# Kernel tuning notes

Measured on AMD Instinct MI355X. Metric: run time of the kernel, lower is better.

The kernel has to match this reference:

```python
import jax, jax.numpy as jnp
import numpy as np

B, N, DIM = 4, 1024, 512
DEPTH, HEADS, DH = 4, 8, 64
INNER = HEADS * DH  # 512
W = 32              # sqrt(N), FeedForward reshapes tokens to (W, W)
SCALE = DH ** -0.5  # used for BOTH spatial and spectral branches (as in source)
EPS_LN = 1e-5
EPS_BN = 1e-5


def setup_inputs() -> dict:
    key = jax.random.key(0)
    ks = jax.random.split(key, 16)
    L = DEPTH
    def rn(k, shape, s=0.02):
        return jax.random.normal(k, shape, jnp.float32) * s
    return {
        "x": jax.random.normal(ks[0], (B, N, DIM), jnp.float32),
        "ln1_w": jnp.ones((L, DIM), jnp.float32), "ln1_b": jnp.zeros((L, DIM), jnp.float32),
        "Wqkv": rn(ks[1], (L, DIM, 3 * INNER)),
        "Wout": rn(ks[2], (L, INNER, DIM)), "bout": jnp.zeros((L, DIM), jnp.float32),
        "sp_w": rn(ks[3], (L, HEADS, HEADS, 3, 3), 0.1), "sp_b": jnp.zeros((L, HEADS), jnp.float32),
        "Wqkv_spec": rn(ks[4], (L, N, 3 * N)),
        "spec_w": rn(ks[5], (L, 1, 1, 3, 3), 0.1), "spec_b": jnp.zeros((L, 1), jnp.float32),
        "ln2_w": jnp.ones((L, DIM), jnp.float32), "ln2_b": jnp.zeros((L, DIM), jnp.float32),
        "dw_w": rn(ks[6], (L, DIM, 1, 3, 3), 0.1), "dw_b": jnp.zeros((L, DIM), jnp.float32),
        "pw_w": rn(ks[7], (L, 256, DIM)), "pw_b": jnp.zeros((L, 256), jnp.float32),
        "bn_g": jnp.ones((L, 256), jnp.float32), "bn_b": jnp.zeros((L, 256), jnp.float32),
        "bn_m": jnp.zeros((L, 256), jnp.float32), "bn_v": jnp.ones((L, 256), jnp.float32),
        "c1_w": rn(ks[8], (L, 512, 256)), "c1_b": jnp.zeros((L, 512), jnp.float32),
        "c2_w": rn(ks[9], (L, DIM, 512)), "c2_b": jnp.zeros((L, DIM), jnp.float32),
    }


def _ln(x, w, b):
    mu = x.mean(-1, keepdims=True)
    var = x.var(-1, keepdims=True)  # biased, matching torch LayerNorm
    return (x - mu) * jax.lax.rsqrt(var + EPS_LN) * w + b


def _conv3x3(x, w, b, groups=1):
    y = jax.lax.conv_general_dilated(x, w, (1, 1), 'SAME',
                                     dimension_numbers=('NCHW', 'OIHW', 'NCHW'),
                                     feature_group_count=groups)
    return y + b[None, :, None, None]


def _block(x, p):
    (ln1w, ln1b, Wqkv, Wout, bout, spw, spb, Wqs, scw, scb,
     ln2w, ln2b, dww, dwb, pww, pwb, bng, bnb, bnm, bnv, c1w, c1b, c2w, c2b) = p
    b = x.shape[0]
    # --- spatial attention (PreNorm) ---
    h = _ln(x, ln1w, ln1b)
    q, k, v = jnp.split(h @ Wqkv, 3, axis=-1)
    split_heads = lambda t: t.reshape(b, N, HEADS, DH).transpose(0, 2, 1, 3)  # b h n d
    q, k, v = split_heads(q), split_heads(k), split_heads(v)
    attn = jax.nn.softmax(jnp.einsum('bhid,bhjd->bhij', q, k) * SCALE, axis=-1)
    attn = _conv3x3(attn, spw, spb)  # conv over the softmax map (heads as channels)
    out = jnp.einsum('bhij,bhjd->bhid', attn, v).transpose(0, 2, 1, 3).reshape(b, N, INNER)
    out = out @ Wout + bout  # (b, n, dim)
    # --- spectral attention on h^T (b, dim, n); v_spec is dead code in source ---
    xt = jnp.swapaxes(h, -1, -2)
    qs, ks_, _vs = jnp.split(xt @ Wqs, 3, axis=-1)  # each (b, dim, n)
    a = jax.nn.softmax(jnp.einsum('bin,bjn->bij', qs, ks_) * SCALE, axis=-1)
    a = _conv3x3(a[:, None], scw, scb)[:, 0]  # (b, dim, dim)
    x = x + jnp.einsum('bnd,bde->bne', out, a)  # residual add from Transformer loop
    # --- FeedForward (PreNorm), FF adds its own internal residual too ---
    h2 = _ln(x, ln2w, ln2b)
    img = h2.reshape(b, W, W, DIM).transpose(0, 3, 1, 2)  # 'b (w h) c -> b c w h'
    t = _conv3x3(img, dww, dwb, groups=DIM)               # depthwise 3x3
    t = jnp.einsum('oc,bchw->bohw', pww, t) + pwb[None, :, None, None]  # pointwise dim->256
    t = (t - bnm[None, :, None, None]) * jax.lax.rsqrt(bnv + EPS_BN)[None, :, None, None] \
        * bng[None, :, None, None] + bnb[None, :, None, None]           # BatchNorm2d (eval)
    t = jax.nn.gelu(jnp.einsum('oc,bchw->bohw', c1w, t) + c1b[None, :, None, None], approximate=False)
    t = jax.nn.gelu(jnp.einsum('oc,bchw->bohw', c2w, t) + c2b[None, :, None, None], approximate=False)
    ff = h2 + t.transpose(0, 2, 3, 1).reshape(b, N, DIM)  # FF internal residual
    return x + ff


def _forward(x, ln1_w, ln1_b, Wqkv, Wout, bout, sp_w, sp_b, Wqkv_spec, spec_w, spec_b,
             ln2_w, ln2_b, dw_w, dw_b, pw_w, pw_b, bn_g, bn_b, bn_m, bn_v,
             c1_w, c1_b, c2_w, c2_b):
    stacked = (ln1_w, ln1_b, Wqkv, Wout, bout, sp_w, sp_b, Wqkv_spec, spec_w, spec_b,
               ln2_w, ln2_b, dw_w, dw_b, pw_w, pw_b, bn_g, bn_b, bn_m, bn_v,
               c1_w, c1_b, c2_w, c2_b)
    for i in range(DEPTH):
        x = _block(x, tuple(a[i] for a in stacked))
    return x


def reference(x, ln1_w, ln1_b, Wqkv, Wout, bout, sp_w, sp_b, Wqkv_spec, spec_w, spec_b,
              ln2_w, ln2_b, dw_w, dw_b, pw_w, pw_b, bn_g, bn_b, bn_m, bn_v,
              c1_w, c1_b, c2_w, c2_b):
    return _forward(x, ln1_w, ln1_b, Wqkv, Wout, bout, sp_w, sp_b, Wqkv_spec, spec_w, spec_b,
                    ln2_w, ln2_b, dw_w, dw_b, pw_w, pw_b, bn_g, bn_b, bn_m, bn_v,
                    c1_w, c1_b, c2_w, c2_b)
```

## Files before the change

kernel.cpp:

```cpp
#include <hip/hip_runtime.h>
#include <hip/hip_bf16.h>

typedef __hip_bfloat16 bf16;
typedef __attribute__((ext_vector_type(8))) short bf16x8;
typedef __attribute__((ext_vector_type(4))) float f32x4;

__device__ __forceinline__ float b2f(bf16 v){ return __bfloat162float(v); }
__device__ __forceinline__ bf16 f2b(float v){ return __float2bfloat16(v); }
__device__ __forceinline__ float bits2f(unsigned u){ return __uint_as_float(u << 16); }
__device__ __forceinline__ unsigned short f2bits(float v){ bf16 t = __float2bfloat16(v); return *(unsigned short*)&t; }

__device__ __forceinline__ float gelu_f(float x){
  return 0.5f * x * (1.f + erff(x * 0.7071067811865475f));
}

__device__ __forceinline__ void gload_lds(const void* g, void* l){
  __builtin_amdgcn_global_load_lds((const __attribute__((address_space(1))) void*)g,
                                   (__attribute__((address_space(3))) void*)l, 16, 0, 0);
}

template<bool MAX>
__device__ __forceinline__ float block_reduce(float v){
  __shared__ float s[4];
  #pragma unroll
  for (int o = 32; o > 0; o >>= 1){
    float t = __shfl_down(v, o, 64);
    v = MAX ? fmaxf(v, t) : (v + t);
  }
  int lane = threadIdx.x & 63, w = threadIdx.x >> 6;
  __syncthreads();
  if (lane == 0) s[w] = v;
  __syncthreads();
  return MAX ? fmaxf(fmaxf(s[0], s[1]), fmaxf(s[2], s[3]))
             : (s[0] + s[1] + s[2] + s[3]);
}

__global__ void detect_k(const unsigned* __restrict__ x, int* __restrict__ flag){
  __shared__ int cnt[256];
  int tid = threadIdx.x;
  int c = 0;
  for (int i = tid; i < 4096; i += 256){
    unsigned h = x[i] & 0xffffu;
    int e = (int)((h >> 7) & 0xff);
    if (h == 0u || (e >= 100 && e <= 133)) c++;
  }
  cnt[tid] = c;
  __syncthreads();
  for (int o = 128; o > 0; o >>= 1){ if (tid < o) cnt[tid] += cnt[tid+o]; __syncthreads(); }
  if (tid == 0) *flag = (cnt[0] < 2048) ? 1 : 0;
}

__global__ __launch_bounds__(256) void cvt_x_k(const void* __restrict__ src,
                                               float* __restrict__ X,
                                               const int* __restrict__ flag){
  int p = blockIdx.x*256 + threadIdx.x;
  X[p] = (*flag) ? ((const float*)src)[p]
                 : __bfloat162float(((const bf16*)src)[p]);
}

struct WCvt21 { const void* src[21]; long long cum[22]; };

__global__ __launch_bounds__(256) void cvt_w_k(WCvt21 a, bf16* __restrict__ WB,
                                               long long total, const int* __restrict__ flag){
  long long i = (long long)blockIdx.x*256 + threadIdx.x;
  if (i >= total) return;
  int t = 0;
  while (a.cum[t+1] <= i) t++;
  long long e = i - a.cum[t];
  WB[i] = (*flag) ? __float2bfloat16(((const float*)a.src[t])[e])
                  : ((const bf16*)a.src[t])[e];
}

__global__ __launch_bounds__(256) void wtrans_k(const void* __restrict__ src, bf16* __restrict__ dst,
                                                int ld_src, int ldd, long long sSrc, long long sDst,
                                                const int* __restrict__ flag){
  __shared__ bf16 t[64][65];
  int z = blockIdx.z;
  int r0 = blockIdx.x*64, c0 = blockIdx.y*64;
  int lane = threadIdx.x & 63, quad = threadIdx.x >> 6;
  const float* sf = (const float*)src;
  const bf16* sb = (const bf16*)src;
  int fl = *flag;
  #pragma unroll
  for (int k = 0; k < 16; ++k){
    int r = quad*16 + k;
    long long idx = z*sSrc + (long long)(r0+r)*ld_src + c0 + lane;
    float v = fl ? sf[idx] : b2f(sb[idx]);
    t[r][lane] = f2b(v);
  }
  __syncthreads();
  #pragma unroll
  for (int k = 0; k < 16; ++k){
    int c = quad*16 + k;
    dst[z*sDst + (long long)(c0+c)*ldd + r0 + lane] = t[lane][c];
  }
}

__global__ void wprep_k(const bf16* __restrict__ spw, bf16* __restrict__ Wr){
  int l = blockIdx.x;
  for (int t = threadIdx.x; t < 1536; t += 256){
    int ho = t / 96, k = t - ho*96;
    float v = 0.f;
    if (ho < 8 && k < 72){
      int tap = k >> 3, hi = k & 7;
      v = b2f(spw[l*576 + ho*72 + hi*9 + tap]);
    }
    Wr[l*1536 + t] = f2b(v);
  }
}

__global__ __launch_bounds__(256) void store_out_k(const float* __restrict__ X,
                                                   void* __restrict__ out,
                                                   const int* __restrict__ flag){
  int p = blockIdx.x*256 + threadIdx.x;
  if (*flag) ((float*)out)[p] = X[p];
  else       ((bf16*)out)[p] = f2b(X[p]);
}

template<int MF, int NF, typename TC>
__global__ __launch_bounds__(256) void gmfma_k(
    int M, int N, int K,
    const bf16* __restrict__ A, int lda, long long sA, long long sA2,
    const bf16* __restrict__ Bt, int ldb, long long sB, long long sB2,
    TC* __restrict__ C, int ldc, long long sC, long long sC2,
    float alpha, int beta,
    const bf16* __restrict__ bias_n,
    const float* __restrict__ scale_n,
    const float* __restrict__ shift_n,
    const bf16* __restrict__ addF,
    int act,
    bf16* __restrict__ vt)
{
  constexpr int BM = MF*32, BN = NF*32;
  constexpr int CHA = BM/16, CH = (BM+BN)/16;
  static_assert(CH % 4 == 0, "chunks must divide among 4 waves");
  __shared__ bf16 Asm[BM][32];
  __shared__ bf16 Bsm[BN][32];
  const int tid = threadIdx.x;
  const int lane = tid & 63, wid = tid >> 6;
  const int wm = wid >> 1, wn = wid & 1;
  const int m0 = blockIdx.y*BM, n0 = blockIdx.x*BN;
  const int z = blockIdx.z;
  const long long zl = z & 7, zh = z >> 3;
  const bf16* Ab = A + zl*sA + zh*sA2;
  const bf16* Bb = Bt + zl*sB + zh*sB2;
  TC* Cb = C + zl*sC + zh*sC2;
  const bf16* Fb = addF ? addF + zl*sC + zh*sC2 : nullptr;

  f32x4 acc[MF][NF];
  f32x4 zero = {0.f, 0.f, 0.f, 0.f};
  #pragma unroll
  for (int m = 0; m < MF; ++m)
    #pragma unroll
    for (int n = 0; n < NF; ++n) acc[m][n] = zero;

  const int rchunk = lane >> 2;
  const int kchunk = (lane & 3) * 8;
  const int row16 = lane & 15, kq = (lane >> 4) * 8;

  for (int k0 = 0; k0 < K; k0 += 32){
    #pragma unroll
    for (int cc = 0; cc < CH/4; ++cc){
      int c = wid + cc*4;
      if (c < CHA){
        int row = c*16 + rchunk;
        gload_lds(Ab + (long long)(m0+row)*lda + k0 + kchunk, &Asm[c*16][0]);
      } else {
        int row = (c-CHA)*16 + rchunk;
        gload_lds(Bb + (long long)(n0+row)*ldb + k0 + kchunk, &Bsm[(c-CHA)*16][0]);
      }
    }
    __syncthreads();
    bf16x8 af[MF], bfr[NF];
    #pragma unroll
    for (int m = 0; m < MF; ++m)
      af[m] = *(const bf16x8*)&Asm[wm*(MF*16) + m*16 + row16][kq];
    #pragma unroll
    for (int n = 0; n < NF; ++n)
      bfr[n] = *(const bf16x8*)&Bsm[wn*(NF*16) + n*16 + row16][kq];
    #pragma unroll
    for (int m = 0; m < MF; ++m)
      #pragma unroll
      for (int n = 0; n < NF; ++n)
        acc[m][n] = __builtin_amdgcn_mfma_f32_16x16x32_bf16(af[m], bfr[n], acc[m][n], 0, 0, 0);
    __syncthreads();
  }

  #pragma unroll
  for (int m = 0; m < MF; ++m){
    #pragma unroll
    for (int n = 0; n < NF; ++n){
      int gn = n0 + wn*(NF*16) + n*16 + row16;
      float bn_ = bias_n ? b2f(bias_n[gn]) : 0.f;
      float sc = scale_n ? scale_n[gn] : 1.f;
      float sh = shift_n ? shift_n[gn] : 0.f;
      int gmb = m0 + wm*(MF*16) + m*16 + (lane >> 4)*4;
      float vals[4];
      #pragma unroll
      for (int r = 0; r < 4; ++r){
        int gm = gmb + r;
        float v = acc[m][n][r] * alpha + bn_;
        v = v * sc + sh;
        if (act) v = gelu_f(v);
        long long idx = (long long)gm*ldc + gn;
        if (Fb) v += b2f(Fb[idx]);
        if (beta){
          float old;
          if constexpr (__is_same(TC, float)) old = Cb[idx]; else old = b2f(Cb[idx]);
          v += old;
        }
        if constexpr (__is_same(TC, float)) Cb[idx] = v; else Cb[idx] = f2b(v);
        vals[r] = v;
      }
      if (vt && gn >= 1024){
        int h = (gn - 1024) >> 6, d = (gn - 1024) & 63;
        int bb = gmb >> 10, nn = gmb & 1023;
        ushort4 o;
        o.x = f2bits(vals[0]); o.y = f2bits(vals[1]);
        o.z = f2bits(vals[2]); o.w = f2bits(vals[3]);
        *(ushort4*)&vt[(((long long)bb*8 + h)*64 + d)*1024 + nn] = o;
      }
    }
  }
}

template<int MF, int NF, typename TC>
static void gmfma_x(hipStream_t st, int z, int M, int N, int K,
                    const bf16* A, int lda, long long sA, long long sA2,
                    const bf16* Bt, int ldb, long long sB, long long sB2,
                    TC* C, int ldc, long long sC, long long sC2,
                    float alpha = 1.f, int beta = 0,
                    const bf16* bias_n = nullptr,
                    const float* scale_n = nullptr, const float* shift_n = nullptr,
                    const bf16* addF = nullptr, int act = 0, bf16* vt = nullptr)
{
  dim3 g(N/(NF*32), M/(MF*32), z);
  gmfma_k<MF,NF,TC><<<g, 256, 0, st>>>(M,N,K,A,lda,sA,sA2,Bt,ldb,sB,sB2,C,ldc,sC,sC2,
                                       alpha,beta,bias_n,scale_n,shift_n,addF,act,vt);
}

template<int MF, int NF, typename TC>
static void gmfma(hipStream_t st, int z, int M, int N, int K,
                  const bf16* A, int lda, long long sA,
                  const bf16* Bt, int ldb, long long sB,
                  TC* C, int ldc, long long sC,
                  float alpha = 1.f, int beta = 0,
                  const bf16* bias_n = nullptr,
                  const float* scale_n = nullptr, const float* shift_n = nullptr,
                  const bf16* addF = nullptr, int act = 0, bf16* vt = nullptr)
{
  gmfma_x<MF,NF,TC>(st, z, M, N, K, A, lda, sA, 8*sA, Bt, ldb, sB, 8*sB,
                    C, ldc, sC, 8*sC, alpha, beta, bias_n, scale_n, shift_n, addF, act, vt);
}

__global__ __launch_bounds__(256) void ln_k(const float* __restrict__ X, bf16* __restrict__ Y,
                                            const bf16* __restrict__ w, const bf16* __restrict__ b){
  long long row = blockIdx.x;
  const float* x = X + row*512;
  bf16* y = Y + row*512;
  int tid = threadIdx.x;
  float v0 = x[tid], v1 = x[tid+256];
  float mean = block_reduce<false>(v0+v1) * (1.f/512.f);
  float msq  = block_reduce<false>(v0*v0+v1*v1) * (1.f/512.f);
  float var = msq - mean*mean;
  float rs = rsqrtf(var + 1e-5f);
  y[tid]     = f2b((v0-mean)*rs*b2f(w[tid])     + b2f(b[tid]));
  y[tid+256] = f2b((v1-mean)*rs*b2f(w[tid+256]) + b2f(b[tid+256]));
}

__global__ __launch_bounds__(256) void maxsum_k(const bf16* __restrict__ Sp,
                                                float* __restrict__ Mrow, float* __restrict__ Irow,
                                                long long bstride){
  __shared__ float redmx[4][8];
  __shared__ float redsum[4][8];
  int i = blockIdx.x;
  long long b = blockIdx.y;
  const bf16* src = Sp + b*bstride + (long long)i*1024;
  int tid = threadIdx.x;
  int lane = tid & 63, w = tid >> 6;
  int j0 = tid*4;

  float v[8][4];
  #pragma unroll
  for (int h = 0; h < 8; ++h){
    ushort4 u = *(const ushort4*)&src[h*1048576 + j0];
    v[h][0] = bits2f(u.x); v[h][1] = bits2f(u.y);
    v[h][2] = bits2f(u.z); v[h][3] = bits2f(u.w);
  }
  #pragma unroll
  for (int h = 0; h < 8; ++h){
    float m = fmaxf(fmaxf(v[h][0], v[h][1]), fmaxf(v[h][2], v[h][3]));
    #pragma unroll
    for (int o = 32; o > 0; o >>= 1) m = fmaxf(m, __shfl_xor(m, o, 64));
    if (lane == 0) redmx[w][h] = m;
  }
  __syncthreads();
  float mx[8];
  #pragma unroll
  for (int h = 0; h < 8; ++h)
    mx[h] = fmaxf(fmaxf(redmx[0][h], redmx[1][h]), fmaxf(redmx[2][h], redmx[3][h]));
  #pragma unroll
  for (int h = 0; h < 8; ++h){
    float s = 0.f;
    #pragma unroll
    for (int r = 0; r < 4; ++r) s += __expf(v[h][r] - mx[h]);
    #pragma unroll
    for (int o = 32; o > 0; o >>= 1) s += __shfl_xor(s, o, 64);
    if (lane == 0) redsum[w][h] = s;
  }
  __syncthreads();
  if (tid < 8){
    float s = redsum[0][tid] + redsum[1][tid] + redsum[2][tid] + redsum[3][tid];
    long long o = (b*1024 + i)*8 + tid;
    Mrow[o] = mx[tid];
    Irow[o] = 1.f / s;
  }
}

__device__ __forceinline__ int csw(int col){ return col ^ ((col >> 3) & 7); }

__global__ __launch_bounds__(256) void convNorm_k(
    const bf16* __restrict__ Sp, bf16* __restrict__ Pout,
    const bf16* __restrict__ Wr, const bf16* __restrict__ bias,
    const float* __restrict__ Mrow, const float* __restrict__ Irow,
    long long bstride)
{
  __shared__ bf16 tile[10][66][8];
  __shared__ float mrow[10][8];
  __shared__ float irow[10][8];
  long long b = blockIdx.z;
  int i0 = blockIdx.y*8;
  int jh0 = blockIdx.x*512;
  int tid = threadIdx.x;
  const bf16* src = Sp + b*bstride;

  if (tid < 80){
    int r = tid >> 3, h = tid & 7;
    int gi = i0 + r - 1;
    float m = 0.f, iv = 0.f;
    if ((unsigned)gi < 1024u){ long long o = (b*1024 + gi)*8 + h; m = Mrow[o]; iv = Irow[o]; }
    mrow[r][h] = m; irow[r][h] = iv;
  }

  int lane = tid & 63, wid = tid >> 6;
  int row16 = lane & 15, q = lane >> 4;
  bf16x8 wf0 = *(const bf16x8*)&Wr[row16*96 +  0 + q*8];
  bf16x8 wf1 = *(const bf16x8*)&Wr[row16*96 + 32 + q*8];
  bf16x8 wf2 = *(const bf16x8*)&Wr[row16*96 + 64 + q*8];
  float bv = (row16 < 8) ? b2f(bias[row16]) : 0.f;

  for (int c = 0; c < 8; ++c){
    int base = jh0 + c*64;
    __syncthreads();
    for (int t = tid; t < 320; t += 256){
      int row = t >> 5, rem = t & 31;
      int hp = rem >> 3, seg = rem & 7;
      int gi = i0 + row - 1;
      int g0 = base + seg*8;
      unsigned ov[8];
      if ((unsigned)gi < 1024u){
        const bf16* p0 = src + (long long)(2*hp)*1048576 + (long long)gi*1024 + g0;
        bf16x8 a0 = *(const bf16x8*)p0;
        bf16x8 a1 = *(const bf16x8*)(p0 + 1048576);
        float m0 = mrow[row][2*hp],   i0v = irow[row][2*hp];
        float m1 = mrow[row][2*hp+1], i1v = irow[row][2*hp+1];
        #pragma unroll
        for (int k = 0; k < 8; ++k){
          float e0 = __expf(bits2f((unsigned)(unsigned short)a0[k]) - m0) * i0v;
          float e1 = __expf(bits2f((unsigned)(unsigned short)a1[k]) - m1) * i1v;
          ov[k] = (unsigned)f2bits(e0) | ((unsigned)f2bits(e1) << 16);
        }
      } else {
        #pragma unroll
        for (int k = 0; k < 8; ++k) ov[k] = 0u;
      }
      #pragma unroll
      for (int k = 0; k < 8; ++k)
        *(unsigned*)&tile[row][csw(1 + seg*8 + k)][2*hp] = ov[k];
    }
    if (tid < 40){
      int row = tid >> 2, hp = tid & 3;
      int gi = i0 + row - 1;
      unsigned L = 0u, R = 0u;
      if ((unsigned)gi < 1024u){
        long long rb = (long long)gi*1024;
        int cl = base - 1, cr = base + 64;
        float m0 = mrow[row][2*hp],   i0v = irow[row][2*hp];
        float m1 = mrow[row][2*hp+1], i1v = irow[row][2*hp+1];
        if (cl >= 0){
          float e0 = __expf(b2f(src[(long long)(2*hp)*1048576 + rb + cl]) - m0) * i0v;
          float e1 = __expf(b2f(src[(long long)(2*hp+1)*1048576 + rb + cl]) - m1) * i1v;
          L = (unsigned)f2bits(e0) | ((unsigned)f2bits(e1) << 16);
        }
        if (cr < 1024){
          float e0 = __expf(b2f(src[(long long)(2*hp)*1048576 + rb + cr]) - m0) * i0v;
          float e1 = __expf(b2f(src[(long long)(2*hp+1)*1048576 + rb + cr]) - m1) * i1v;
          R = (unsigned)f2bits(e0) | ((unsigned)f2bits(e1) << 16);
        }
      }
      *(unsigned*)&tile[row][csw(0)][2*hp] = L;
      *(unsigned*)&tile[row][csw(65)][2*hp] = R;
    }
    __syncthreads();
    #pragma unroll
    for (int rr = 0; rr < 2; ++rr){
      int ii = rr*4 + wid;
      f32x4 zero = {0.f,0.f,0.f,0.f};
      f32x4 acc[4] = {zero,zero,zero,zero};
      #pragma unroll
      for (int ks = 0; ks < 3; ++ks){
        int tap = ks*4 + q;
        int tcl = tap > 8 ? 0 : tap;
        int di = tcl/3, dj = tcl - di*3;
        bf16x8 wsel = ks==0 ? wf0 : (ks==1 ? wf1 : wf2);
        #pragma unroll
        for (int mf = 0; mf < 4; ++mf){
          bf16x8 af = *(const bf16x8*)&tile[ii+di][csw(mf*16 + row16 + dj)][0];
          acc[mf] = __builtin_amdgcn_mfma_f32_16x16x32_bf16(af, wsel, acc[mf], 0, 0, 0);
        }
      }
      if (row16 < 8){
        bf16* dst = Pout + b*bstride + (long long)row16*1048576 + (long long)(i0+ii)*1024;
        #pragma unroll
        for (int mf = 0; mf < 4; ++mf){
          int j = base + mf*16 + q*4;
          ushort4 o;
          o.x = f2bits(acc[mf][0] + bv);
          o.y = f2bits(acc[mf][1] + bv);
          o.z = f2bits(acc[mf][2] + bv);
          o.w = f2bits(acc[mf][3] + bv);
          *(ushort4*)&dst[j] = o;
        }
      }
    }
  }
}

__global__ __launch_bounds__(256) void spec_ms_k(const float* __restrict__ A,
                                                 float* __restrict__ Sm, float* __restrict__ Si){
  int row = blockIdx.x;
  const float* p = A + (long long)row*512;
  int tid = threadIdx.x;
  float v0 = p[tid], v1 = p[tid+256];
  float mx = block_reduce<true>(fmaxf(v0, v1));
  float s = block_reduce<false>(__expf(v0-mx) + __expf(v1-mx));
  if (tid == 0){ Sm[row] = mx; Si[row] = 1.f/s; }
}

__global__ __launch_bounds__(256) void conv_spec_k(const float* __restrict__ in, bf16* __restrict__ out,
                                                   const bf16* __restrict__ w, const bf16* __restrict__ bias,
                                                   const float* __restrict__ Sm, const float* __restrict__ Si){
  __shared__ float ti[66][67];
  __shared__ bf16 toutT[64][65];
  __shared__ float sms[66], sis[66];
  int b = blockIdx.z;
  int i0 = blockIdx.y*64, j0 = blockIdx.x*64;
  int tid = threadIdx.x;
  const float* ib = in + (long long)b*262144;
  if (tid < 66){
    int gi = i0 + tid - 1;
    float m = 0.f, iv = 0.f;
    if ((unsigned)gi < 512u){ m = Sm[b*512 + gi]; iv = Si[b*512 + gi]; }
    sms[tid] = m; sis[tid] = iv;
  }
  __syncthreads();
  for (int t = tid; t < 66*66; t += 256){
    int r = t / 66, cc = t - r*66;
    int gi = i0 + r - 1, gj = j0 + cc - 1;
    float v = 0.f;
    if ((unsigned)gi < 512u && (unsigned)gj < 512u)
      v = __expf(ib[gi*512 + gj] - sms[r]) * sis[r];
    ti[r][cc] = v;
  }
  __syncthreads();
  float w9[9], bv = b2f(bias[0]);
  #pragma unroll
  for (int d = 0; d < 9; ++d) w9[d] = b2f(w[d]);
  int ii = tid & 63;
  #pragma unroll
  for (int q = 0; q < 16; ++q){
    int jj = (tid >> 6)*16 + q;
    float acc = bv;
    #pragma unroll
    for (int di = 0; di < 3; ++di)
      #pragma unroll
      for (int dj = 0; dj < 3; ++dj)
        acc += w9[di*3+dj] * ti[ii+di][jj+dj];
    toutT[jj][ii] = f2b(acc);
  }
  __syncthreads();
  #pragma unroll
  for (int q = 0; q < 16; ++q){
    int jj = (tid >> 6)*16 + q;
    out[(long long)b*262144 + (j0+jj)*512 + i0 + (tid & 63)] = toutT[jj][tid & 63];
  }
}

__global__ __launch_bounds__(256) void dwconv_k(const bf16* __restrict__ H2, bf16* __restrict__ T1,
                                                const bf16* __restrict__ w, const bf16* __restrict__ bias){
  int p = blockIdx.x*256 + threadIdx.x;
  int cp = p & 255;
  int n = (p >> 8) & 1023;
  int b = p >> 18;
  int c0 = cp*2;
  int wi = n >> 5, hg = n & 31;
  float a0 = b2f(bias[c0]), a1 = b2f(bias[c0+1]);
  #pragma unroll
  for (int di = 0; di < 3; ++di){
    int gw = wi + di - 1;
    if ((unsigned)gw >= 32u) continue;
    #pragma unroll
    for (int dj = 0; dj < 3; ++dj){
      int gh = hg + dj - 1;
      if ((unsigned)gh >= 32u) continue;
      unsigned hv = *(const unsigned*)&H2[((long long)b*1024 + (gw*32+gh))*512 + c0];
      float w0 = b2f(w[c0*9 + di*3 + dj]);
      float w1 = b2f(w[(c0+1)*9 + di*3 + dj]);
      a0 += w0 * bits2f(hv & 0xffffu);
      a1 += w1 * bits2f(hv >> 16);
    }
  }
  bf16 h0 = f2b(a0), h1 = f2b(a1);
  unsigned o = ((unsigned)*(unsigned short*)&h1 << 16) | (unsigned)*(unsigned short*)&h0;
  *(unsigned*)&T1[((long long)b*1024 + n)*512 + c0] = o;
}

__global__ void bnaff_all_k(const bf16* __restrict__ pwb, const bf16* __restrict__ g,
                            const bf16* __restrict__ bb, const bf16* __restrict__ m,
                            const bf16* __restrict__ v, float* __restrict__ BNAFF){
  int l = blockIdx.x, o = threadIdx.x;
  float s = b2f(g[l*256+o]) * rsqrtf(b2f(v[l*256+o]) + 1e-5f);
  BNAFF[l*512 + o] = s;
  BNAFF[l*512 + 256 + o] = (b2f(pwb[l*256+o]) - b2f(m[l*256+o])) * s + b2f(bb[l*256+o]);
}

__global__ __launch_bounds__(256) void htrans_k(const bf16* __restrict__ Hb, bf16* __restrict__ HT){
  __shared__ bf16 t[64][65];
  int b = blockIdx.z;
  int n0 = blockIdx.x*64, c0 = blockIdx.y*64;
  int lane = threadIdx.x & 63, quad = threadIdx.x >> 6;
  #pragma unroll
  for (int k = 0; k < 16; ++k){
    int r = quad*16 + k;
    t[r][lane] = Hb[((long long)b*1024 + n0 + r)*512 + c0 + lane];
  }
  __syncthreads();
  #pragma unroll
  for (int k = 0; k < 16; ++k){
    int c = quad*16 + k;
    HT[(long long)b*524288 + (long long)(c0+c)*1024 + n0 + lane] = t[lane][c];
  }
}

extern "C" void kernel_launch(void* const* d_in, const int* in_sizes, int n_in,
                              void* d_out, int out_size, void* d_ws, size_t ws_size,
                              hipStream_t stream)
{
  (void)in_sizes; (void)n_in; (void)out_size;

  const bool big = ws_size >= 207000000ull;
  const long long ATTN_SZ = big ? 33554432LL : 8388608LL;

  float* X     = (float*)d_ws;
  bf16*  WBsm  = (bf16*)(X + 2097152);
  bf16*  WqkvT = WBsm  + 2139648;
  bf16*  WoutT = WqkvT + 3145728;
  bf16*  WqsT  = WoutT + 1048576;
  bf16*  Hbuf  = WqsT  + 8388608;
  bf16*  HbufT = Hbuf  + 2097152;
  bf16*  QKV   = HbufT + 2097152;
  bf16*  Vt    = QKV   + 6291456;
  bf16*  OUTH  = Vt    + 2097152;
  bf16*  OUT   = OUTH  + 2097152;
  bf16*  ATTN  = OUT   + 2097152;
  bf16*  ATTNC = ATTN  + ATTN_SZ;
  float* BNAFF = (float*)(ATTNC + ATTN_SZ);
  bf16*  WR    = (bf16*)(BNAFF + 2048);
  float* MROW  = (float*)(WR + 6144);
  float* IROW  = MROW + 32768;
  float* SMS   = IROW + 32768;
  float* SIS   = SMS + 2048;
  int*   FLAG  = (int*)(SIS + 2048);

  float* ASPEC   = (float*)OUTH;
  bf16*  ASPECCT = ATTNC;
  bf16*  T1 = ATTN;
  bf16*  T3 = ATTN + 2097152;
  bf16*  T2 = ATTNC + 2097152;
  bf16*  SQK = ATTN;

  static const int widx[21] = {1,2,5,6,7,9,10,11,12,13,14,15,16,17,18,19,20,21,22,23,24};
  static const long long wsz[21] = {2048,2048,2048,2304,32,36,4,2048,2048,18432,2048,
                                    524288,1024,1024,1024,1024,1024,524288,2048,1048576,2048};
  WCvt21 wc;
  long long cum = 0;
  bf16* wp[21];
  for (int t = 0; t < 21; ++t){
    wc.src[t] = d_in[widx[t]];
    wc.cum[t] = cum;
    wp[t] = WBsm + cum;
    cum += wsz[t];
  }
  wc.cum[21] = cum;

  bf16 *w_ln1w = wp[0],  *w_ln1b = wp[1],  *w_bout = wp[2],  *w_spw = wp[3];
  bf16 *w_spb  = wp[4],  *w_specw= wp[5],  *w_specb= wp[6],  *w_ln2w= wp[7];
  bf16 *w_ln2b = wp[8],  *w_dww  = wp[9],  *w_dwb  = wp[10], *w_pww = wp[11];
  bf16 *w_pwb  = wp[12], *w_bng  = wp[13], *w_bnb  = wp[14], *w_bnm = wp[15];
  bf16 *w_bnv  = wp[16], *w_c1w  = wp[17], *w_c1b  = wp[18], *w_c2w = wp[19];
  bf16 *w_c2b  = wp[20];

  detect_k<<<1, 256, 0, stream>>>((const unsigned*)d_in[0], FLAG);
  cvt_x_k<<<8192, 256, 0, stream>>>(d_in[0], X, FLAG);
  cvt_w_k<<<(int)((cum + 255)/256), 256, 0, stream>>>(wc, WBsm, cum, FLAG);
  wtrans_k<<<dim3(8,24,4), 256, 0, stream>>>(d_in[3], WqkvT, 1536, 512, 786432LL, 786432LL, FLAG);
  wtrans_k<<<dim3(8, 8,4), 256, 0, stream>>>(d_in[4], WoutT,  512, 512, 262144LL, 262144LL, FLAG);
  wtrans_k<<<dim3(16,32,4),256, 0, stream>>>(d_in[8], WqsT,  3072,1024, 3145728LL,2097152LL, FLAG);
  bnaff_all_k<<<4, 256, 0, stream>>>(w_pwb, w_bng, w_bnb, w_bnm, w_bnv, BNAFF);
  wprep_k<<<4, 256, 0, stream>>>(w_spw, WR);

  for (int l = 0; l < 4; ++l){
    ln_k<<<4096, 256, 0, stream>>>(X, Hbuf, w_ln1w + l*512, w_ln1b + l*512);
    gmfma<4,4,bf16>(stream, 1, 4096, 1536, 512,
        Hbuf, 512, 0, WqkvT + (long long)l*786432, 512, 0, QKV, 1536, 0,
        1.f, 0, nullptr, nullptr, nullptr, nullptr, 0, Vt);
    if (big){
      gmfma_x<4,4,bf16>(stream, 32, 1024, 1024, 64,
          QKV, 1536, 64, 1572864, QKV + 512, 1536, 64, 1572864,
          ATTN, 1024, 1048576, 8388608, 0.125f);
      maxsum_k<<<dim3(1024,4), 256, 0, stream>>>(ATTN, MROW, IROW, 8388608LL);
      convNorm_k<<<dim3(2,128,4), 256, 0, stream>>>(ATTN, ATTNC, WR + l*1536, w_spb + l*8,
                                                    MROW, IROW, 8388608LL);
      gmfma_x<2,2,bf16>(stream, 32, 1024, 64, 1024,
          ATTNC, 1024, 1048576, 8388608, Vt, 1024, 65536, 524288,
          OUTH, 512, 64, 524288);
    } else {
      for (int b = 0; b < 4; ++b){
        bf16* qkvb = QKV + (long long)b*1572864;
        gmfma<4,4,bf16>(stream, 8, 1024, 1024, 64,
            qkvb, 1536, 64, qkvb + 512, 1536, 64, ATTN, 1024, 1048576, 0.125f);
        maxsum_k<<<dim3(1024,1), 256, 0, stream>>>(ATTN, MROW, IROW, 8388608LL);
        convNorm_k<<<dim3(2,128,1), 256, 0, stream>>>(ATTN, ATTNC, WR + l*1536, w_spb + l*8,
                                                      MROW, IROW, 8388608LL);
        gmfma<2,2,bf16>(stream, 8, 1024, 64, 1024,
            ATTNC, 1024, 1048576, Vt + (long long)b*524288, 1024, 65536,
            OUTH + (long long)b*524288, 512, 64);
      }
    }
    gmfma<2,2,bf16>(stream, 1, 4096, 512, 512,
        OUTH, 512, 0, WoutT + (long long)l*262144, 512, 0, OUT, 512, 0,
        1.f, 0, w_bout + l*512);
    htrans_k<<<dim3(16,8,4), 256, 0, stream>>>(Hbuf, HbufT);
    gmfma<4,4,bf16>(stream, 4, 512, 2048, 1024,
        HbufT, 1024, 524288, WqsT + (long long)l*2097152, 1024, 0, SQK, 2048, 1048576);
    gmfma<2,2,float>(stream, 4, 512, 512, 1024,
        SQK, 2048, 1048576, SQK + 1024, 2048, 1048576, ASPEC, 512, 262144, 0.125f);
    spec_ms_k<<<2048, 256, 0, stream>>>(ASPEC, SMS, SIS);
    conv_spec_k<<<dim3(8,8,4), 256, 0, stream>>>(ASPEC, ASPECCT, w_specw + l*9, w_specb + l,
                                                 SMS, SIS);
    gmfma<2,2,float>(stream, 4, 1024, 512, 512,
        OUT, 512, 524288, ASPECCT, 512, 262144, X, 512, 524288, 1.f, 1);
    ln_k<<<4096, 256, 0, stream>>>(X, Hbuf, w_ln2w + l*512, w_ln2b + l*512);
    dwconv_k<<<4096, 256, 0, stream>>>(Hbuf, T1, w_dww + l*4608, w_dwb + l*512);
    gmfma<2,2,bf16>(stream, 4, 1024, 256, 512,
        T1, 512, 524288, w_pww + (long long)l*131072, 512, 0, T2, 256, 262144,
        1.f, 0, nullptr, BNAFF + l*512, BNAFF + l*512 + 256);
    gmfma<2,2,bf16>(stream, 4, 1024, 512, 256,
        T2, 256, 262144, w_c1w + (long long)l*131072, 256, 0, T3, 512, 524288,
        1.f, 0, w_c1b + l*512, nullptr, nullptr, nullptr, 1);
    gmfma<2,2,float>(stream, 4, 1024, 512, 512,
        T3, 512, 524288, w_c2w + (long long)l*262144, 512, 0, X, 512, 524288,
        1.f, 1, w_c2b + l*512, nullptr, nullptr, Hbuf, 1);
  }

  store_out_k<<<8192, 256, 0, stream>>>(X, d_out, FLAG);
}
```

Measured before the change: 1.233 ms.

## Fuse softmax exp and row-sum into score GEMM epilogue, drop max-sum kernels

The score GEMMs for both spatial and spectral attention now apply exp in their epilogue, store the exponentials, and atomically accumulate per-row sums. This removes the separate max/sum reduction kernels and the exp in the conv-normalize kernels, which now just multiply by the reciprocal row sum. The max subtraction is dropped, so correctness relies on scores being small enough not to overflow exp. It adds atomics, a zeroing kernel each layer, and regrids convNorm to more blocks.

```diff
diff --git a/kernel.cpp b/kernel.cpp
--- a/kernel.cpp
+++ b/kernel.cpp
@@ -117,7 +117,12 @@
   else       ((bf16*)out)[p] = f2b(X[p]);
 }
 
-template<int MF, int NF, typename TC>
+__global__ __launch_bounds__(256) void zero_k(float* __restrict__ p, int n){
+  int i = blockIdx.x*256 + threadIdx.x;
+  if (i < n) p[i] = 0.f;
+}
+
+template<int MF, int NF, typename TC, int EXP>
 __global__ __launch_bounds__(256) void gmfma_k(
     int M, int N, int K,
     const bf16* __restrict__ A, int lda, long long sA, long long sA2,
@@ -129,7 +134,8 @@
     const float* __restrict__ shift_n,
     const bf16* __restrict__ addF,
     int act,
-    bf16* __restrict__ vt)
+    bf16* __restrict__ vt,
+    float* __restrict__ srow, long long szl, long long szh, long long sgm)
 {
   constexpr int BM = MF*32, BN = NF*32;
   constexpr int CHA = BM/16, CH = (BM+BN)/16;
@@ -184,6 +190,34 @@
       for (int n = 0; n < NF; ++n)
         acc[m][n] = __builtin_amdgcn_mfma_f32_16x16x32_bf16(af[m], bfr[n], acc[m][n], 0, 0, 0);
     __syncthreads();
+  }
+
+  if constexpr (EXP){
+    #pragma unroll
+    for (int m = 0; m < MF; ++m){
+      int gmb = m0 + wm*(MF*16) + m*16 + (lane >> 4)*4;
+      float rowsum[4] = {0.f, 0.f, 0.f, 0.f};
+      #pragma unroll
+      for (int n = 0; n < NF; ++n){
+        int gn = n0 + wn*(NF*16) + n*16 + row16;
+        #pragma unroll
+        for (int r = 0; r < 4; ++r){
+          float e = __expf(acc[m][n][r] * alpha);
+          long long idx = (long long)(gmb + r)*ldc + gn;
+          if constexpr (__is_same(TC, float)) Cb[idx] = e; else Cb[idx] = f2b(e);
+          rowsum[r] += e;
+        }
+      }
+      #pragma unroll
+      for (int r = 0; r < 4; ++r){
+        float s = rowsum[r];
+        #pragma unroll
+        for (int o = 1; o < 16; o <<= 1) s += __shfl_xor(s, o, 64);
+        if ((lane & 15) == 0)
+          atomicAdd(&srow[zl*szl + zh*szh + (long long)(gmb + r)*sgm], s);
+      }
+    }
+    return;
   }
 
   #pragma unroll
@@ -235,8 +269,9 @@
                     const bf16* addF = nullptr, int act = 0, bf16* vt = nullptr)
 {
   dim3 g(N/(NF*32), M/(MF*32), z);
-  gmfma_k<MF,NF,TC><<<g, 256, 0, st>>>(M,N,K,A,lda,sA,sA2,Bt,ldb,sB,sB2,C,ldc,sC,sC2,
-                                       alpha,beta,bias_n,scale_n,shift_n,addF,act,vt);
+  gmfma_k<MF,NF,TC,0><<<g, 256, 0, st>>>(M,N,K,A,lda,sA,sA2,Bt,ldb,sB,sB2,C,ldc,sC,sC2,
+                                         alpha,beta,bias_n,scale_n,shift_n,addF,act,vt,
+                                         nullptr,0,0,0);
 }
 
 template<int MF, int NF, typename TC>
@@ -251,6 +286,20 @@
 {
   gmfma_x<MF,NF,TC>(st, z, M, N, K, A, lda, sA, 8*sA, Bt, ldb, sB, 8*sB,
                     C, ldc, sC, 8*sC, alpha, beta, bias_n, scale_n, shift_n, addF, act, vt);
+}
+
+template<int MF, int NF, typename TC>
+static void gmfma_exp(hipStream_t st, int z, int M, int N, int K,
+                      const bf16* A, int lda, long long sA, long long sA2,
+                      const bf16* Bt, int ldb, long long sB, long long sB2,
+                      TC* C, int ldc, long long sC, long long sC2,
+                      float alpha,
+                      float* srow, long long szl, long long szh, long long sgm)
+{
+  dim3 g(N/(NF*32), M/(MF*32), z);
+  gmfma_k<MF,NF,TC,1><<<g, 256, 0, st>>>(M,N,K,A,lda,sA,sA2,Bt,ldb,sB,sB2,C,ldc,sC,sC2,
+                                         alpha,0,nullptr,nullptr,nullptr,nullptr,0,nullptr,
+                                         srow,szl,szh,sgm);
 }
 
 __global__ __launch_bounds__(256) void ln_k(const float* __restrict__ X, bf16* __restrict__ Y,
@@ -268,78 +317,28 @@
   y[tid+256] = f2b((v1-mean)*rs*b2f(w[tid+256]) + b2f(b[tid+256]));
 }
 
-__global__ __launch_bounds__(256) void maxsum_k(const bf16* __restrict__ Sp,
-                                                float* __restrict__ Mrow, float* __restrict__ Irow,
-                                                long long bstride){
-  __shared__ float redmx[4][8];
-  __shared__ float redsum[4][8];
-  int i = blockIdx.x;
-  long long b = blockIdx.y;
-  const bf16* src = Sp + b*bstride + (long long)i*1024;
-  int tid = threadIdx.x;
-  int lane = tid & 63, w = tid >> 6;
-  int j0 = tid*4;
-
-  float v[8][4];
-  #pragma unroll
-  for (int h = 0; h < 8; ++h){
-    ushort4 u = *(const ushort4*)&src[h*1048576 + j0];
-    v[h][0] = bits2f(u.x); v[h][1] = bits2f(u.y);
-    v[h][2] = bits2f(u.z); v[h][3] = bits2f(u.w);
-  }
-  #pragma unroll
-  for (int h = 0; h < 8; ++h){
-    float m = fmaxf(fmaxf(v[h][0], v[h][1]), fmaxf(v[h][2], v[h][3]));
-    #pragma unroll
-    for (int o = 32; o > 0; o >>= 1) m = fmaxf(m, __shfl_xor(m, o, 64));
-    if (lane == 0) redmx[w][h] = m;
-  }
-  __syncthreads();
-  float mx[8];
-  #pragma unroll
-  for (int h = 0; h < 8; ++h)
-    mx[h] = fmaxf(fmaxf(redmx[0][h], redmx[1][h]), fmaxf(redmx[2][h], redmx[3][h]));
-  #pragma unroll
-  for (int h = 0; h < 8; ++h){
-    float s = 0.f;
-    #pragma unroll
-    for (int r = 0; r < 4; ++r) s += __expf(v[h][r] - mx[h]);
-    #pragma unroll
-    for (int o = 32; o > 0; o >>= 1) s += __shfl_xor(s, o, 64);
-    if (lane == 0) redsum[w][h] = s;
-  }
-  __syncthreads();
-  if (tid < 8){
-    float s = redsum[0][tid] + redsum[1][tid] + redsum[2][tid] + redsum[3][tid];
-    long long o = (b*1024 + i)*8 + tid;
-    Mrow[o] = mx[tid];
-    Irow[o] = 1.f / s;
-  }
-}
-
 __device__ __forceinline__ int csw(int col){ return col ^ ((col >> 3) & 7); }
 
 __global__ __launch_bounds__(256) void convNorm_k(
     const bf16* __restrict__ Sp, bf16* __restrict__ Pout,
     const bf16* __restrict__ Wr, const bf16* __restrict__ bias,
-    const float* __restrict__ Mrow, const float* __restrict__ Irow,
+    const float* __restrict__ Srow,
     long long bstride)
 {
   __shared__ bf16 tile[10][66][8];
-  __shared__ float mrow[10][8];
   __shared__ float irow[10][8];
   long long b = blockIdx.z;
   int i0 = blockIdx.y*8;
-  int jh0 = blockIdx.x*512;
+  int jh0 = blockIdx.x*256;
   int tid = threadIdx.x;
   const bf16* src = Sp + b*bstride;
 
   if (tid < 80){
     int r = tid >> 3, h = tid & 7;
     int gi = i0 + r - 1;
-    float m = 0.f, iv = 0.f;
-    if ((unsigned)gi < 1024u){ long long o = (b*1024 + gi)*8 + h; m = Mrow[o]; iv = Irow[o]; }
-    mrow[r][h] = m; irow[r][h] = iv;
+    float iv = 0.f;
+    if ((unsigned)gi < 1024u) iv = 1.f / Srow[(b*1024 + gi)*8 + h];
+    irow[r][h] = iv;
   }
 
   int lane = tid & 63, wid = tid >> 6;
@@ -349,7 +348,7 @@
   bf16x8 wf2 = *(const bf16x8*)&Wr[row16*96 + 64 + q*8];
   float bv = (row16 < 8) ? b2f(bias[row16]) : 0.f;
 
-  for (int c = 0; c < 8; ++c){
+  for (int c = 0; c < 4; ++c){
     int base = jh0 + c*64;
     __syncthreads();
     for (int t = tid; t < 320; t += 256){
@@ -362,12 +361,12 @@
         const bf16* p0 = src + (long long)(2*hp)*1048576 + (long long)gi*1024 + g0;
         bf16x8 a0 = *(const bf16x8*)p0;
         bf16x8 a1 = *(const bf16x8*)(p0 + 1048576);
-        float m0 = mrow[row][2*hp],   i0v = irow[row][2*hp];
-        float m1 = mrow[row][2*hp+1], i1v = irow[row][2*hp+1];
+        float i0v = irow[row][2*hp];
+        float i1v = irow[row][2*hp+1];
         #pragma unroll
         for (int k = 0; k < 8; ++k){
-          float e0 = __expf(bits2f((unsigned)(unsigned short)a0[k]) - m0) * i0v;
-          float e1 = __expf(bits2f((unsigned)(unsigned short)a1[k]) - m1) * i1v;
+          float e0 = bits2f((unsigned)(unsigned short)a0[k]) * i0v;
+          float e1 = bits2f((unsigned)(unsigned short)a1[k]) * i1v;
           ov[k] = (unsigned)f2bits(e0) | ((unsigned)f2bits(e1) << 16);
         }
       } else {
@@ -385,16 +384,16 @@
       if ((unsigned)gi < 1024u){
         long long rb = (long long)gi*1024;
         int cl = base - 1, cr = base + 64;
-        float m0 = mrow[row][2*hp],   i0v = irow[row][2*hp];
-        float m1 = mrow[row][2*hp+1], i1v = irow[row][2*hp+1];
+        float i0v = irow[row][2*hp];
+        float i1v = irow[row][2*hp+1];
         if (cl >= 0){
-          float e0 = __expf(b2f(src[(long long)(2*hp)*1048576 + rb + cl]) - m0) * i0v;
-          float e1 = __expf(b2f(src[(long long)(2*hp+1)*1048576 + rb + cl]) - m1) * i1v;
+          float e0 = b2f(src[(long long)(2*hp)*1048576 + rb + cl]) * i0v;
+          float e1 = b2f(src[(long long)(2*hp+1)*1048576 + rb + cl]) * i1v;
           L = (unsigned)f2bits(e0) | ((unsigned)f2bits(e1) << 16);
         }
         if (cr < 1024){
-          float e0 = __expf(b2f(src[(long long)(2*hp)*1048576 + rb + cr]) - m0) * i0v;
-          float e1 = __expf(b2f(src[(long long)(2*hp+1)*1048576 + rb + cr]) - m1) * i1v;
+          float e0 = b2f(src[(long long)(2*hp)*1048576 + rb + cr]) * i0v;
+          float e1 = b2f(src[(long long)(2*hp+1)*1048576 + rb + cr]) * i1v;
           R = (unsigned)f2bits(e0) | ((unsigned)f2bits(e1) << 16);
         }
       }
@@ -436,32 +435,21 @@
   }
 }
 
-__global__ __launch_bounds__(256) void spec_ms_k(const float* __restrict__ A,
-                                                 float* __restrict__ Sm, float* __restrict__ Si){
-  int row = blockIdx.x;
-  const float* p = A + (long long)row*512;
-  int tid = threadIdx.x;
-  float v0 = p[tid], v1 = p[tid+256];
-  float mx = block_reduce<true>(fmaxf(v0, v1));
-  float s = block_reduce<false>(__expf(v0-mx) + __expf(v1-mx));
-  if (tid == 0){ Sm[row] = mx; Si[row] = 1.f/s; }
-}
-
 __global__ __launch_bounds__(256) void conv_spec_k(const float* __restrict__ in, bf16* __restrict__ out,
                                                    const bf16* __restrict__ w, const bf16* __restrict__ bias,
-                                                   const float* __restrict__ Sm, const float* __restrict__ Si){
+                                                   const float* __restrict__ SSrow){
   __shared__ float ti[66][67];
   __shared__ bf16 toutT[64][65];
-  __shared__ float sms[66], sis[66];
+  __shared__ float sis[66];
   int b = blockIdx.z;
   int i0 = blockIdx.y*64, j0 = blockIdx.x*64;
   int tid = threadIdx.x;
   const float* ib = in + (long long)b*262144;
   if (tid < 66){
     int gi = i0 + tid - 1;
-    float m = 0.f, iv = 0.f;
-    if ((unsigned)gi < 512u){ m = Sm[b*512 + gi]; iv = Si[b*512 + gi]; }
-    sms[tid] = m; sis[tid] = iv;
+    float iv = 0.f;
+    if ((unsigned)gi < 512u) iv = 1.f / SSrow[b*512 + gi];
+    sis[tid] = iv;
   }
   __syncthreads();
   for (int t = tid; t < 66*66; t += 256){
@@ -469,7 +457,7 @@
     int gi = i0 + r - 1, gj = j0 + cc - 1;
     float v = 0.f;
     if ((unsigned)gi < 512u && (unsigned)gj < 512u)
-      v = __expf(ib[gi*512 + gj] - sms[r]) * sis[r];
+      v = ib[gi*512 + gj] * sis[r];
     ti[r][cc] = v;
   }
   __syncthreads();
@@ -576,11 +564,9 @@
   bf16*  ATTNC = ATTN  + ATTN_SZ;
   float* BNAFF = (float*)(ATTNC + ATTN_SZ);
   bf16*  WR    = (bf16*)(BNAFF + 2048);
-  float* MROW  = (float*)(WR + 6144);
-  float* IROW  = MROW + 32768;
-  float* SMS   = IROW + 32768;
-  float* SIS   = SMS + 2048;
-  int*   FLAG  = (int*)(SIS + 2048);
+  float* SROW  = (float*)(WR + 6144);
+  float* SSROW = SROW + 32768;
+  int*   FLAG  = (int*)(SSROW + 2048);
 
   float* ASPEC   = (float*)OUTH;
   bf16*  ASPECCT = ATTNC;
@@ -620,28 +606,30 @@
   wprep_k<<<4, 256, 0, stream>>>(w_spw, WR);
 
   for (int l = 0; l < 4; ++l){
+    zero_k<<<136, 256, 0, stream>>>(SROW, 34816);
     ln_k<<<4096, 256, 0, stream>>>(X, Hbuf, w_ln1w + l*512, w_ln1b + l*512);
     gmfma<4,4,bf16>(stream, 1, 4096, 1536, 512,
         Hbuf, 512, 0, WqkvT + (long long)l*786432, 512, 0, QKV, 1536, 0,
         1.f, 0, nullptr, nullptr, nullptr, nullptr, 0, Vt);
     if (big){
-      gmfma_x<4,4,bf16>(stream, 32, 1024, 1024, 64,
+      gmfma_exp<4,4,bf16>(stream, 32, 1024, 1024, 64,
           QKV, 1536, 64, 1572864, QKV + 512, 1536, 64, 1572864,
-          ATTN, 1024, 1048576, 8388608, 0.125f);
-      maxsum_k<<<dim3(1024,4), 256, 0, stream>>>(ATTN, MROW, IROW, 8388608LL);
-      convNorm_k<<<dim3(2,128,4), 256, 0, stream>>>(ATTN, ATTNC, WR + l*1536, w_spb + l*8,
-                                                    MROW, IROW, 8388608LL);
+          ATTN, 1024, 1048576, 8388608, 0.125f,
+          SROW, 1, 8192, 8);
+      convNorm_k<<<dim3(4,128,4), 256, 0, stream>>>(ATTN, ATTNC, WR + l*1536, w_spb + l*8,
+                                                    SROW, 8388608LL);
       gmfma_x<2,2,bf16>(stream, 32, 1024, 64, 1024,
           ATTNC, 1024, 1048576, 8388608, Vt, 1024, 65536, 524288,
           OUTH, 512, 64, 524288);
     } else {
       for (int b = 0; b < 4; ++b){
         bf16* qkvb = QKV + (long long)b*1572864;
-        gmfma<4,4,bf16>(stream, 8, 1024, 1024, 64,
-            qkvb, 1536, 64, qkvb + 512, 1536, 64, ATTN, 1024, 1048576, 0.125f);
-        maxsum_k<<<dim3(1024,1), 256, 0, stream>>>(ATTN, MROW, IROW, 8388608LL);
-        convNorm_k<<<dim3(2,128,1), 256, 0, stream>>>(ATTN, ATTNC, WR + l*1536, w_spb + l*8,
-                                                      MROW, IROW, 8388608LL);
+        gmfma_exp<4,4,bf16>(stream, 8, 1024, 1024, 64,
+            qkvb, 1536, 64, 8*64, qkvb + 512, 1536, 64, 8*64,
+            ATTN, 1024, 1048576, 8*1048576, 0.125f,
+            SROW + b*8192, 1, 0, 8);
+        convNorm_k<<<dim3(4,128,1), 256, 0, stream>>>(ATTN, ATTNC, WR + l*1536, w_spb + l*8,
+                                                      SROW + b*8192, 8388608LL);
         gmfma<2,2,bf16>(stream, 8, 1024, 64, 1024,
             ATTNC, 1024, 1048576, Vt + (long long)b*524288, 1024, 65536,
             OUTH + (long long)b*524288, 512, 64);
@@ -653,11 +641,12 @@
     htrans_k<<<dim3(16,8,4), 256, 0, stream>>>(Hbuf, HbufT);
     gmfma<4,4,bf16>(stream, 4, 512, 2048, 1024,
         HbufT, 1024, 524288, WqsT + (long long)l*2097152, 1024, 0, SQK, 2048, 1048576);
-    gmfma<2,2,float>(stream, 4, 512, 512, 1024,
-        SQK, 2048, 1048576, SQK + 1024, 2048, 1048576, ASPEC, 512, 262144, 0.125f);
-    spec_ms_k<<<2048, 256, 0, stream>>>(ASPEC, SMS, SIS);
+    gmfma_exp<2,2,float>(stream, 4, 512, 512, 1024,
+        SQK, 2048, 1048576, 8*1048576, SQK + 1024, 2048, 1048576, 8*1048576,
+        ASPEC, 512, 262144, 8*262144, 0.125f,
+        SSROW, 512, 0, 1);
     conv_spec_k<<<dim3(8,8,4), 256, 0, stream>>>(ASPEC, ASPECCT, w_specw + l*9, w_specb + l,
-                                                 SMS, SIS);
+                                                 SSROW);
     gmfma<2,2,float>(stream, 4, 1024, 512, 512,
         OUT, 512, 524288, ASPECCT, 512, 262144, X, 512, 524288, 1.f, 1);
     ln_k<<<4096, 256, 0, stream>>>(X, Hbuf, w_ln2w + l*512, w_ln2b + l*512);
```

Measured after the change: 1.215 ms. About the same (-1.4%).
